# Kernel tuning notes

Measured on AMD Instinct MI355X. Metric: run time of the kernel, lower is better.

Reference implementation:

```python
import jax, jax.numpy as jnp
import numpy as np

EMBED_DIM = 1024
NUM_HEADS = 16
HEAD_DIM = EMBED_DIM // NUM_HEADS
TGT_LEN, BSZ = 2048, 4


def setup_inputs() -> dict:
    key = jax.random.key(0)
    ks = jax.random.split(key, 12)
    s = 1.0 / np.sqrt(EMBED_DIM)
    inp = {
        "query": jax.random.normal(ks[0], (TGT_LEN, BSZ, EMBED_DIM), jnp.float32),
        "key": jax.random.normal(ks[1], (TGT_LEN, BSZ, EMBED_DIM), jnp.float32),
        "value": jax.random.normal(ks[2], (TGT_LEN, BSZ, EMBED_DIM), jnp.float32),
        # nn.Linear weights: [out, in], y = x @ W.T + b
        "Wq": jax.random.normal(ks[3], (EMBED_DIM, EMBED_DIM), jnp.float32) * s,
        "bq": jax.random.normal(ks[4], (EMBED_DIM,), jnp.float32) * s,
        "Wk": jax.random.normal(ks[5], (EMBED_DIM, EMBED_DIM), jnp.float32) * s,
        "bk": jax.random.normal(ks[6], (EMBED_DIM,), jnp.float32) * s,
        "Wv": jax.random.normal(ks[7], (EMBED_DIM, EMBED_DIM), jnp.float32) * s,
        "bv": jax.random.normal(ks[8], (EMBED_DIM,), jnp.float32) * s,
        "Wo": jax.random.normal(ks[9], (EMBED_DIM, EMBED_DIM), jnp.float32) * s,
        "bo": jax.random.normal(ks[10], (EMBED_DIM,), jnp.float32) * s,
    }
    return inp


def _split_heads(x, seq_len, bsz):
    # [S, B, E] -> [B*H, S, Dh]
    return x.reshape(seq_len, bsz * NUM_HEADS, HEAD_DIM).transpose(1, 0, 2)


def reference(query, key, value, Wq, bq, Wk, bk, Wv, bv, Wo, bo):
    tgt_len, bsz, embed_dim = query.shape
    src_len = key.shape[0]
    q = query @ Wq.T + bq
    k = key @ Wk.T + bk
    v = value @ Wv.T + bv
    q = _split_heads(q, tgt_len, bsz)   # [B*H, T, Dh]
    k = _split_heads(k, src_len, bsz)   # [B*H, S, Dh]
    v = _split_heads(v, src_len, bsz)   # [B*H, S, Dh]
    scale = 1.0 / np.sqrt(HEAD_DIM).astype(np.float32)
    attn_weights = jnp.einsum('btd,bsd->bts', q, k) * scale  # [B*H, T, S]
    attn_weights = jax.nn.softmax(attn_weights, axis=-1)
    attn = jnp.einsum('bts,bsd->btd', attn_weights, v)       # [B*H, T, Dh]
    attn = attn.transpose(1, 0, 2).reshape(tgt_len, bsz, embed_dim)
    return attn @ Wo.T + bo
```

## Files before the change

### kernel.cpp

```cpp
#include <hip/hip_runtime.h>
#include <stdint.h>

#define TGT 2048
#define BSZQ 4
#define EMB 1024
#define NHEAD 16
#define DH 64
#define BH 64
#define MROWS 8192

using short8 = __attribute__((ext_vector_type(8))) short;
using f32x4  = __attribute__((ext_vector_type(4))) float;
typedef unsigned short u16;
typedef unsigned int u32;

#define QSCALE 0.18033688011112042f

__device__ __forceinline__ u16 f2bf(float f) {
  union { float f; u32 u; } v; v.f = f;
  return (u16)((v.u + 0x7fffu + ((v.u >> 16) & 1u)) >> 16);
}
__device__ __forceinline__ u32 packbf(float a, float b) {
  union { float f; u32 u; } x, y; x.f = a; y.f = b;
  return __builtin_amdgcn_perm(y.u + 0x8000u, x.u + 0x8000u, 0x07060302u);
}
__device__ __forceinline__ f32x4 mfma16(short8 a, short8 b, f32x4 c) {
  return __builtin_amdgcn_mfma_f32_16x16x32_bf16(a, b, c, 0, 0, 0);
}
__device__ __forceinline__ void gload_lds16(const u16* g, u16* l) {
  __builtin_amdgcn_global_load_lds((const __attribute__((address_space(1))) void*)g,
                                   (__attribute__((address_space(3))) void*)l,
                                   16, 0, 0);
}

__global__ __launch_bounds__(256)
void cvt3(const float* __restrict__ a, const float* __restrict__ b, const float* __restrict__ c,
          u16* __restrict__ oa, u16* __restrict__ ob, u16* __restrict__ oc)
{
  const float* s; u16* d;
  if (blockIdx.y == 0) { s = a; d = oa; }
  else if (blockIdx.y == 1) { s = b; d = ob; }
  else { s = c; d = oc; }
  const int i = (blockIdx.x * 256 + threadIdx.x) * 8;
  float4 v0 = *(const float4*)(s + i);
  float4 v1 = *(const float4*)(s + i + 4);
  union { u16 h[8]; short8 v; } r;
  r.h[0] = f2bf(v0.x); r.h[1] = f2bf(v0.y); r.h[2] = f2bf(v0.z); r.h[3] = f2bf(v0.w);
  r.h[4] = f2bf(v1.x); r.h[5] = f2bf(v1.y); r.h[6] = f2bf(v1.z); r.h[7] = f2bf(v1.w);
  *(short8*)(d + i) = r.v;
}
__global__ __launch_bounds__(256)
void cvt4(const float* __restrict__ a, const float* __restrict__ b,
          const float* __restrict__ c, const float* __restrict__ e,
          u16* __restrict__ oa, u16* __restrict__ ob, u16* __restrict__ oc, u16* __restrict__ oe)
{
  const float* s; u16* d;
  if (blockIdx.y == 0) { s = a; d = oa; }
  else if (blockIdx.y == 1) { s = b; d = ob; }
  else if (blockIdx.y == 2) { s = c; d = oc; }
  else { s = e; d = oe; }
  const int i = (blockIdx.x * 256 + threadIdx.x) * 8;
  float4 v0 = *(const float4*)(s + i);
  float4 v1 = *(const float4*)(s + i + 4);
  union { u16 h[8]; short8 v; } r;
  r.h[0] = f2bf(v0.x); r.h[1] = f2bf(v0.y); r.h[2] = f2bf(v0.z); r.h[3] = f2bf(v0.w);
  r.h[4] = f2bf(v1.x); r.h[5] = f2bf(v1.y); r.h[6] = f2bf(v1.z); r.h[7] = f2bf(v1.w);
  *(short8*)(d + i) = r.v;
}

__device__ __forceinline__
void gemm_body(const u16* __restrict__ A, const u16* __restrict__ W,
               const float* __restrict__ bias, void* __restrict__ outp,
               u16* As, u16* Bs, int mode, int m0, int n0)
{
  const int tid = threadIdx.x;
  const int wave = tid >> 6, lane = tid & 63;
  const int col16 = lane & 15, quad = lane >> 4;
  const int wr = (wave >> 1) * 64;
  const int wc = (wave & 1) * 64;
  const int sr16 = lane & 15;
  const int sl = lane >> 4;
  const int akb = (wave >> 1) * 4;
  const int bkb = (wave & 1) * 4;

#define GSTAGE(K0, CB) do { \
  _Pragma("unroll") for (int s_ = 0; s_ < 2; ++s_) { \
    const int t_ = wave * 2 + s_; \
    gload_lds16(A + (size_t)(m0 + t_ * 16 + sr16) * EMB + (K0) + sl * 8, \
                &As[(CB) * 4096 + t_ * 512]); \
    gload_lds16(W + (size_t)(n0 + t_ * 16 + sr16) * EMB + (K0) + sl * 8, \
                &Bs[(CB) * 4096 + t_ * 512]); \
  } } while (0)

  f32x4 acc[4][4];
#pragma unroll
  for (int i = 0; i < 4; ++i)
#pragma unroll
    for (int j = 0; j < 4; ++j) acc[i][j] = (f32x4)0.0f;

  GSTAGE(0, 0);
  for (int kt = 0; kt < EMB / 32; ++kt) {
    const int cb = kt & 1;
    __syncthreads();
    if (kt < EMB / 32 - 1) GSTAGE((kt + 1) * 32, cb ^ 1);
    short8 af[4], bfr[4];
#pragma unroll
    for (int i = 0; i < 4; ++i)
      af[i] = *(const short8*)&As[cb * 4096 + (akb + i) * 512 + quad * 128 + col16 * 8];
#pragma unroll
    for (int j = 0; j < 4; ++j)
      bfr[j] = *(const short8*)&Bs[cb * 4096 + (bkb + j) * 512 + quad * 128 + col16 * 8];
#pragma unroll
    for (int i = 0; i < 4; ++i)
#pragma unroll
      for (int j = 0; j < 4; ++j)
        acc[i][j] = mfma16(af[i], bfr[j], acc[i][j]);
  }
#undef GSTAGE

  const int rowb = quad * 4;
#pragma unroll
  for (int i = 0; i < 4; ++i) {
#pragma unroll
    for (int j = 0; j < 4; ++j) {
      const int gn = n0 + wc + j * 16 + col16;
      const float bia = bias[gn];
      const int h = gn >> 6, d = gn & 63;
#pragma unroll
      for (int r = 0; r < 4; ++r) {
        const int gm = m0 + wr + i * 16 + rowb + r;
        float val = acc[i][j][r] + bia;
        const int t = gm >> 2, b = gm & 3;
        if (mode == 0) {
          ((u16*)outp)[((size_t)(b * NHEAD + h) * TGT + t) * DH + d] = f2bf(val * QSCALE);
        } else if (mode == 1) {
          ((u16*)outp)[((size_t)(b * NHEAD + h) * TGT + t) * DH + d] = f2bf(val);
        } else if (mode == 2) {
          const int p = (t & ~63) + ((t & 12) << 2) + ((t & 48) >> 2) + (t & 3);
          ((u16*)outp)[((size_t)(b * NHEAD + h) * DH + d) * TGT + p] = f2bf(val);
        } else {
          ((float*)outp)[(size_t)gm * EMB + gn] = val;
        }
      }
    }
  }
}

__global__ __launch_bounds__(256, 4)
void gemm_qkv(const u16* __restrict__ qb, const u16* __restrict__ kb, const u16* __restrict__ vb,
              const u16* __restrict__ wq, const u16* __restrict__ wk, const u16* __restrict__ wv,
              const float* __restrict__ bq, const float* __restrict__ bk, const float* __restrict__ bv,
              u16* __restrict__ qh, u16* __restrict__ kh, u16* __restrict__ vtp)
{
  __shared__ u16 As[2 * 4096];
  __shared__ u16 Bs[2 * 4096];
  const int lin = ((int)blockIdx.z * 64 + blockIdx.y) * 8 + blockIdx.x;
  const int swz = (lin & 7) * 192 + (lin >> 3);
  const int n0 = (swz & 7) * 128;
  const int tmp = swz >> 3;
  const int m0 = (tmp & 63) * 128;
  const int z = tmp >> 6;
  const u16* A = (z == 0) ? qb : (z == 1) ? kb : vb;
  const u16* W = (z == 0) ? wq : (z == 1) ? wk : wv;
  const float* bias = (z == 0) ? bq : (z == 1) ? bk : bv;
  void* outp = (z == 0) ? (void*)qh : (z == 1) ? (void*)kh : (void*)vtp;
  gemm_body(A, W, bias, outp, As, Bs, z, m0, n0);
}

__global__ __launch_bounds__(256, 4)
void gemm_o(const u16* __restrict__ A, const u16* __restrict__ W,
            const float* __restrict__ bias, float* __restrict__ outp)
{
  __shared__ u16 As[2 * 4096];
  __shared__ u16 Bs[2 * 4096];
  const int lin = (int)blockIdx.y * 8 + blockIdx.x;
  const int swz = (lin & 7) * 64 + (lin >> 3);
  const int n0 = (swz & 7) * 128;
  const int m0 = (swz >> 3) * 128;
  gemm_body(A, W, bias, (void*)outp, As, Bs, 3, m0, n0);
}

__global__ __launch_bounds__(256, 4)
void flash_attn(const u16* __restrict__ qh, const u16* __restrict__ kh,
                const u16* __restrict__ vtp, u16* __restrict__ ao)
{
  __shared__ u16 Ks[2 * 64 * 64];
  __shared__ u16 Vs[2 * 64 * 64];

  const int tid = threadIdx.x;
  const int wave = tid >> 6, lane = tid & 63;
  const int col16 = lane & 15, quad = lane >> 4;
  const int id = blockIdx.x;
  const int bh = (id & 7) * 8 + (id >> 7);
  const int q0 = ((id >> 3) & 15) * 128;
  const int wq0 = q0 + wave * 32;

  const u16* qbase = qh + (size_t)bh * TGT * DH;
  const u16* kbase = kh + (size_t)bh * TGT * DH;
  const u16* vbase = vtp + (size_t)bh * DH * TGT;

  const int krl = lane >> 3;
  const int kgl = (lane & 7) ^ krl;

#define STAGE(S0, B) do { \
  _Pragma("unroll") for (int t_ = 0; t_ < 2; ++t_) { \
    gload_lds16(kbase + (size_t)((S0) + t_ * 32 + wave * 8 + krl) * DH + kgl * 8, \
                &Ks[(B) * 4096 + (t_ * 32 + wave * 8) * 64]); \
    gload_lds16(vbase + (size_t)(t_ * 32 + wave * 8 + krl) * TGT + (S0) + kgl * 8, \
                &Vs[(B) * 4096 + (t_ * 32 + wave * 8) * 64]); \
  } } while (0)

  short8 qf[2][2];
#pragma unroll
  for (int i = 0; i < 2; ++i)
#pragma unroll
    for (int kk = 0; kk < 2; ++kk)
      qf[i][kk] = *(const short8*)(qbase + (size_t)(wq0 + i * 16 + col16) * DH + kk * 32 + quad * 8);

  f32x4 oacc[2][4];
  float lsum[2];
#pragma unroll
  for (int i = 0; i < 2; ++i) {
    lsum[i] = 0.0f;
#pragma unroll
    for (int j = 0; j < 4; ++j) oacc[i][j] = (f32x4)0.0f;
  }

  STAGE(0, 0);

  for (int st = 0; st < TGT / 64; ++st) {
    const int cb = st & 1;
    __syncthreads();
    if (st < TGT / 64 - 1) STAGE((st + 1) * 64, cb ^ 1);

    u32 pka[4][2][2];
#pragma unroll
    for (int j = 0; j < 4; ++j) {
      const int R = j * 16 + col16;
      short8 kf0 = *(const short8*)&Ks[cb * 4096 + R * 64 + ((quad ^ (col16 & 7)) << 3)];
      short8 kf1 = *(const short8*)&Ks[cb * 4096 + R * 64 + (((quad + 4) ^ (col16 & 7)) << 3)];
#pragma unroll
      for (int i = 0; i < 2; ++i) {
        f32x4 t0 = mfma16(kf0, qf[i][0], (f32x4)0.0f);
        f32x4 s  = mfma16(kf1, qf[i][1], t0);
        float p0 = __builtin_amdgcn_exp2f(s[0]);
        float p1 = __builtin_amdgcn_exp2f(s[1]);
        float p2 = __builtin_amdgcn_exp2f(s[2]);
        float p3 = __builtin_amdgcn_exp2f(s[3]);
        lsum[i] += (p0 + p1) + (p2 + p3);
        pka[j][i][0] = packbf(p0, p1);
        pka[j][i][1] = packbf(p2, p3);
      }
    }
#pragma unroll
    for (int jd = 0; jd < 4; ++jd) {
      const int d = jd * 16 + col16;
#pragma unroll
      for (int h = 0; h < 2; ++h) {
        short8 vf = *(const short8*)&Vs[cb * 4096 + d * 64
                                        + (((quad * 2 + h) ^ (d & 7)) << 3)];
#pragma unroll
        for (int i = 0; i < 2; ++i) {
          union { u32 u[4]; short8 s8; } pa;
          pa.u[0] = pka[2 * h][i][0];     pa.u[1] = pka[2 * h][i][1];
          pa.u[2] = pka[2 * h + 1][i][0]; pa.u[3] = pka[2 * h + 1][i][1];
          oacc[i][jd] = mfma16(pa.s8, vf, oacc[i][jd]);
        }
      }
    }
  }
#undef STAGE

  float lrow[2][4];
#pragma unroll
  for (int i = 0; i < 2; ++i) {
    float L = lsum[i];
    L += __shfl_xor(L, 16, 64);
    L += __shfl_xor(L, 32, 64);
    L = __builtin_amdgcn_rcpf(L);
#pragma unroll
    for (int r = 0; r < 4; ++r) lrow[i][r] = __shfl(L, quad * 4 + r, 64);
  }
  const int b = bh >> 4, h = bh & 15;
#pragma unroll
  for (int i = 0; i < 2; ++i)
#pragma unroll
    for (int jd = 0; jd < 4; ++jd)
#pragma unroll
      for (int r = 0; r < 4; ++r) {
        const int t = q0 + wave * 32 + i * 16 + quad * 4 + r;
        const int d = jd * 16 + col16;
        ao[((size_t)t * BSZQ + b) * EMB + h * DH + d] = f2bf(oacc[i][jd][r] * lrow[i][r]);
      }
}

extern "C" void kernel_launch(void* const* d_in, const int* in_sizes, int n_in,
                              void* d_out, int out_size, void* d_ws, size_t ws_size,
                              hipStream_t stream) {
  const float* query = (const float*)d_in[0];
  const float* key   = (const float*)d_in[1];
  const float* value = (const float*)d_in[2];
  const float* Wq = (const float*)d_in[3];
  const float* bq = (const float*)d_in[4];
  const float* Wk = (const float*)d_in[5];
  const float* bk = (const float*)d_in[6];
  const float* Wv = (const float*)d_in[7];
  const float* bv = (const float*)d_in[8];
  const float* Wo = (const float*)d_in[9];
  const float* bo = (const float*)d_in[10];

  const size_t BIG = (size_t)MROWS * EMB;
  const size_t WSZ = (size_t)EMB * EMB;
  u16* buf0 = (u16*)d_ws;
  u16* buf1 = buf0 + BIG;
  u16* buf2 = buf1 + BIG;
  u16* buf3 = buf2 + BIG;
  u16* wqb  = buf3 + BIG;
  u16* wkb  = wqb + WSZ;
  u16* wvb  = wkb + WSZ;
  u16* wob  = wvb + WSZ;
  u16* khs  = (u16*)d_out;
  u16* vts  = khs + BIG;

  cvt3<<<dim3(BIG / 2048, 3), 256, 0, stream>>>(query, key, value, buf0, buf1, buf2);
  cvt4<<<dim3(WSZ / 2048, 4), 256, 0, stream>>>(Wq, Wk, Wv, Wo, wqb, wkb, wvb, wob);

  gemm_qkv<<<dim3(EMB / 128, MROWS / 128, 3), 256, 0, stream>>>(
      buf0, buf1, buf2, wqb, wkb, wvb, bq, bk, bv,
      buf3 , khs , vts );

  flash_attn<<<1024, 256, 0, stream>>>(buf3, khs, vts, buf2);

  gemm_o<<<dim3(EMB / 128, MROWS / 128), 256, 0, stream>>>(buf2, wob, bo, (float*)d_out);
}
```

Baseline: 404.2 us.

## Load GEMM fragments directly from global memory instead of staging through LDS

The projection GEMMs no longer stage A and W tiles through double-buffered shared memory with barriers. Each wave now reads its MFMA operand fragments straight from global memory through per-row pointers, with the K loop fully unrolled. This removes LDS traffic and __syncthreads, but drops the cross-wave data sharing: each A and B row is now fetched by two waves instead of once per block, so global and L2 traffic rise and load latency is no longer hidden by the explicit prefetch.

```diff
diff --git a/kernel.cpp b/kernel.cpp
--- a/kernel.cpp
+++ b/kernel.cpp
@@ -71,26 +71,21 @@
 __device__ __forceinline__
 void gemm_body(const u16* __restrict__ A, const u16* __restrict__ W,
                const float* __restrict__ bias, void* __restrict__ outp,
-               u16* As, u16* Bs, int mode, int m0, int n0)
+               int mode, int m0, int n0)
 {
   const int tid = threadIdx.x;
   const int wave = tid >> 6, lane = tid & 63;
   const int col16 = lane & 15, quad = lane >> 4;
   const int wr = (wave >> 1) * 64;
   const int wc = (wave & 1) * 64;
-  const int sr16 = lane & 15;
-  const int sl = lane >> 4;
-  const int akb = (wave >> 1) * 4;
-  const int bkb = (wave & 1) * 4;
-
-#define GSTAGE(K0, CB) do { \
-  _Pragma("unroll") for (int s_ = 0; s_ < 2; ++s_) { \
-    const int t_ = wave * 2 + s_; \
-    gload_lds16(A + (size_t)(m0 + t_ * 16 + sr16) * EMB + (K0) + sl * 8, \
-                &As[(CB) * 4096 + t_ * 512]); \
-    gload_lds16(W + (size_t)(n0 + t_ * 16 + sr16) * EMB + (K0) + sl * 8, \
-                &Bs[(CB) * 4096 + t_ * 512]); \
-  } } while (0)
+
+  const u16* rowA[4];
+  const u16* rowB[4];
+#pragma unroll
+  for (int i = 0; i < 4; ++i) {
+    rowA[i] = A + (size_t)(m0 + wr + i * 16 + col16) * EMB + quad * 8;
+    rowB[i] = W + (size_t)(n0 + wc + i * 16 + col16) * EMB + quad * 8;
+  }
 
   f32x4 acc[4][4];
 #pragma unroll
@@ -98,25 +93,19 @@
 #pragma unroll
     for (int j = 0; j < 4; ++j) acc[i][j] = (f32x4)0.0f;
 
-  GSTAGE(0, 0);
+#pragma unroll
   for (int kt = 0; kt < EMB / 32; ++kt) {
-    const int cb = kt & 1;
-    __syncthreads();
-    if (kt < EMB / 32 - 1) GSTAGE((kt + 1) * 32, cb ^ 1);
-    short8 af[4], bfr[4];
+    short8 af[4], bf[4];
+#pragma unroll
+    for (int i = 0; i < 4; ++i) af[i] = *(const short8*)(rowA[i] + kt * 32);
+#pragma unroll
+    for (int j = 0; j < 4; ++j) bf[j] = *(const short8*)(rowB[j] + kt * 32);
 #pragma unroll
     for (int i = 0; i < 4; ++i)
-      af[i] = *(const short8*)&As[cb * 4096 + (akb + i) * 512 + quad * 128 + col16 * 8];
-#pragma unroll
-    for (int j = 0; j < 4; ++j)
-      bfr[j] = *(const short8*)&Bs[cb * 4096 + (bkb + j) * 512 + quad * 128 + col16 * 8];
-#pragma unroll
-    for (int i = 0; i < 4; ++i)
 #pragma unroll
       for (int j = 0; j < 4; ++j)
-        acc[i][j] = mfma16(af[i], bfr[j], acc[i][j]);
-  }
-#undef GSTAGE
+        acc[i][j] = mfma16(af[i], bf[j], acc[i][j]);
+  }
 
   const int rowb = quad * 4;
 #pragma unroll
@@ -152,8 +141,6 @@
               const float* __restrict__ bq, const float* __restrict__ bk, const float* __restrict__ bv,
               u16* __restrict__ qh, u16* __restrict__ kh, u16* __restrict__ vtp)
 {
-  __shared__ u16 As[2 * 4096];
-  __shared__ u16 Bs[2 * 4096];
   const int lin = ((int)blockIdx.z * 64 + blockIdx.y) * 8 + blockIdx.x;
   const int swz = (lin & 7) * 192 + (lin >> 3);
   const int n0 = (swz & 7) * 128;
@@ -164,20 +151,18 @@
   const u16* W = (z == 0) ? wq : (z == 1) ? wk : wv;
   const float* bias = (z == 0) ? bq : (z == 1) ? bk : bv;
   void* outp = (z == 0) ? (void*)qh : (z == 1) ? (void*)kh : (void*)vtp;
-  gemm_body(A, W, bias, outp, As, Bs, z, m0, n0);
+  gemm_body(A, W, bias, outp, z, m0, n0);
 }
 
 __global__ __launch_bounds__(256, 4)
 void gemm_o(const u16* __restrict__ A, const u16* __restrict__ W,
             const float* __restrict__ bias, float* __restrict__ outp)
 {
-  __shared__ u16 As[2 * 4096];
-  __shared__ u16 Bs[2 * 4096];
   const int lin = (int)blockIdx.y * 8 + blockIdx.x;
   const int swz = (lin & 7) * 64 + (lin >> 3);
   const int n0 = (swz & 7) * 128;
   const int m0 = (swz >> 3) * 128;
-  gemm_body(A, W, bias, (void*)outp, As, Bs, 3, m0, n0);
+  gemm_body(A, W, bias, (void*)outp, 3, m0, n0);
 }
 
 __global__ __launch_bounds__(256, 4)
```

Measured after the change: 511.9 us. +26.7%, slower.
